# Kernel tuning notes

Measured on AMD Instinct MI355X. Metric: run time of the kernel, lower is better.

## Reference

```python
import jax, jax.numpy as jnp
import numpy as np

B, N, D_IN = 2, 2048, 256
H, DH = 8, 32  # num_heads, head_dim (out_features=256, concat=True)


def setup_inputs() -> dict:
    key = jax.random.key(0)
    ks = jax.random.split(key, 7)
    s = 1.0 / np.sqrt(D_IN)
    x = jax.random.normal(ks[0], (B, N, D_IN), dtype=jnp.float32)
    adj = jax.random.randint(ks[1], (B, N, N), 0, 2).astype(jnp.float32)
    eye = jnp.eye(N, dtype=jnp.float32)[None]
    adj = jnp.maximum(adj, eye)
    Wq = jax.random.normal(ks[2], (H * DH, D_IN), dtype=jnp.float32) * s
    Wk = jax.random.normal(ks[3], (H * DH, D_IN), dtype=jnp.float32) * s
    Wv = jax.random.normal(ks[4], (H * DH, D_IN), dtype=jnp.float32) * s
    Wo = jax.random.normal(ks[5], (H * DH, H * DH), dtype=jnp.float32) * s
    bo = jnp.zeros((H * DH,), dtype=jnp.float32)
    return {"x": x, "adj": adj, "Wq": Wq, "Wk": Wk, "Wv": Wv, "Wo": Wo, "bo": bo}


def reference(x, adj, Wq, Wk, Wv, Wo, bo):
    b, n, _ = x.shape
    # projections -> (b, h, n, dh)
    Q = (x @ Wq.T).reshape(b, n, H, DH).transpose(0, 2, 1, 3)
    K = (x @ Wk.T).reshape(b, n, H, DH).transpose(0, 2, 1, 3)
    V = (x @ Wv.T).reshape(b, n, H, DH).transpose(0, 2, 1, 3)
    scores = jnp.einsum('bhnd,bhmd->bhnm', Q, K) / jnp.sqrt(jnp.float32(DH))
    mask = (adj[:, None, :, :] == 0)  # (b,1,n,n) broadcast over heads
    scores = jnp.where(mask, -jnp.inf, scores)
    attn = jax.nn.softmax(scores, axis=-1)  # dropout is identity in eval
    out = jnp.einsum('bhnm,bhmd->bhnd', attn, V)
    out = out.transpose(0, 2, 1, 3).reshape(b, n, H * DH)  # concat heads
    return out @ Wo.T + bo
```

## Files before the change

### kernel.cpp

```cpp
#include <hip/hip_runtime.h>
#include <hip/hip_bf16.h>

#define BB   2
#define NNN  2048
#define DIN  256
#define HH   8
#define DHD  32
#define NW   32

typedef __attribute__((ext_vector_type(8))) short short8;
typedef __attribute__((ext_vector_type(4))) float f32x4;
typedef __attribute__((ext_vector_type(16))) float f32x16;

#if __has_builtin(__builtin_amdgcn_exp2f)
#define EXP2(x) __builtin_amdgcn_exp2f(x)
#else
#define EXP2(x) exp2f(x)
#endif

__device__ __forceinline__ unsigned int pk2(float a, float b) {
  union { __hip_bfloat162 h2; unsigned int u; } cv;
  cv.h2 = __float22bfloat162_rn(float2{a, b});
  return cv.u;
}
__device__ __forceinline__ unsigned short f2bf(float f) {
  unsigned int u = __float_as_uint(f);
  u += 0x7fffu + ((u >> 16) & 1u);
  return (unsigned short)(u >> 16);
}

#define QSCALE (0.17677669529663687f * 1.4426950408889634f)

__global__ __launch_bounds__(256) void build_mask(
    const float* __restrict__ adj, unsigned long long* __restrict__ Mk,
    const float* __restrict__ Wo, unsigned short* __restrict__ Wob) {
  const int bid = blockIdx.x, tid = threadIdx.x;
  if (bid < 1024) {
    const int lane = tid & 63;
    const int row = bid * 4 + (tid >> 6);
    const float* rp = adj + (size_t)row * NNN + lane * 4;
    #pragma unroll
    for (int o = 0; o < 2; ++o) {
      float4 vv[4];
      #pragma unroll
      for (int g = 0; g < 4; ++g)
        vv[g] = *(const float4*)(rp + (o * 4 + g) * 256);
      #pragma unroll
      for (int g = 0; g < 4; ++g) {
        unsigned long long b0 = __ballot(vv[g].x != 0.0f);
        unsigned long long b1 = __ballot(vv[g].y != 0.0f);
        unsigned long long b2 = __ballot(vv[g].z != 0.0f);
        unsigned long long b3 = __ballot(vv[g].w != 0.0f);
        if (lane < 4) {
          unsigned long long bs = (lane == 0) ? b0 : (lane == 1) ? b1 : (lane == 2) ? b2 : b3;
          Mk[(size_t)row * NW + (o * 4 + g) * 4 + lane] = bs;
        }
      }
    }
  } else {
    int i = (bid - 1024) * 1024 + tid * 4;
    float4 v = *(const float4*)(Wo + i);
    unsigned int p[2] = {pk2(v.x, v.y), pk2(v.z, v.w)};
    *(uint2*)(Wob + i) = *(const uint2*)p;
  }
}

__global__ __launch_bounds__(256) void qkv_gemm(
    const float* __restrict__ x, const float* __restrict__ Wq,
    const float* __restrict__ Wk, const float* __restrict__ Wv,
    unsigned short* __restrict__ Qb, unsigned short* __restrict__ Kb,
    unsigned short* __restrict__ Vt) {
  __shared__ __align__(16) unsigned short Wl[64][264];
  const int tid = threadIdx.x;
  const int y = blockIdx.x >> 6, rb = blockIdx.x & 63;
  const int mat = y >> 2, ocb = (y & 3) * 64;
  const float* Wsrc = ((mat == 0) ? Wq : (mat == 1) ? Wk : Wv) + (size_t)ocb * DIN;

  #pragma unroll
  for (int it = 0; it < 16; ++it) {
    int f4 = it * 256 + tid;
    int oc = f4 >> 6, k4 = f4 & 63;
    float4 v = *(const float4*)(Wsrc + (size_t)oc * DIN + k4 * 4);
    unsigned int p[2] = {pk2(v.x, v.y), pk2(v.z, v.w)};
    *(uint2*)&Wl[oc][k4 * 4] = *(const uint2*)p;
  }
  __syncthreads();

  const int w = tid >> 6, lane = tid & 63, col = lane & 15, quad = lane >> 4;
  const int row0 = rb * 64 + w * 16;

  f32x4 acc[4];
  #pragma unroll
  for (int c = 0; c < 4; ++c) acc[c] = (f32x4){0.f, 0.f, 0.f, 0.f};

  #pragma unroll
  for (int kk = 0; kk < 8; ++kk) {
    const float* xp = x + (size_t)(row0 + col) * DIN + kk * 32 + quad * 8;
    float4 a0 = *(const float4*)xp, a1 = *(const float4*)(xp + 4);
    union { short8 s; unsigned int u[4]; } af;
    af.u[0] = pk2(a0.x, a0.y); af.u[1] = pk2(a0.z, a0.w);
    af.u[2] = pk2(a1.x, a1.y); af.u[3] = pk2(a1.z, a1.w);
    #pragma unroll
    for (int c = 0; c < 4; ++c) {
      short8 bw = *(const short8*)&Wl[c * 16 + col][kk * 32 + quad * 8];
      acc[c] = __builtin_amdgcn_mfma_f32_16x16x32_bf16(af.s, bw, acc[c], 0, 0, 0);
    }
  }
  const float scale = (mat == 0) ? QSCALE : 1.0f;
  #pragma unroll
  for (int c = 0; c < 4; ++c) {
    int oc = ocb + c * 16 + col, h = oc >> 5, dh = oc & 31;
    #pragma unroll
    for (int r = 0; r < 4; ++r) {
      int row = row0 + quad * 4 + r;
      int b = row >> 11, n = row & (NNN - 1);
      unsigned short val = f2bf(acc[c][r] * scale);
      if (mat == 2)       Vt[((size_t)(b * HH + h) * DHD + dh) * NNN + n] = val;
      else if (mat == 0)  Qb[((size_t)(b * HH + h) * NNN + n) * DHD + dh] = val;
      else                Kb[((size_t)(b * HH + h) * NNN + n) * DHD + dh] = val;
    }
  }
}

__global__ __launch_bounds__(512, 6) void attn(
    const unsigned short* __restrict__ Qb, const unsigned short* __restrict__ Kb,
    const unsigned short* __restrict__ Vt, const unsigned long long* __restrict__ Mk,
    unsigned short* __restrict__ AOb) {
  __shared__ float OL[8][32][33];
  __shared__ float LL[8][32];
  const int tid = threadIdx.x;
  const int w = tid >> 6, lane = tid & 63;
  const int qi = lane & 31, hi = lane >> 5;
  const int bid = blockIdx.x;
  const int xcd = bid & 7, j = bid >> 3;
  const int bh = xcd * 2 + (j >> 6);
  const int qt = j & 63;
  const int b = bh >> 3, h = bh & 7;
  const int q = qt * 32 + qi;
  const int k0 = w * 256;

  const unsigned short* qp = Qb + ((size_t)bh * NNN + q) * DHD + hi * 8;
  const short8 bq0 = *(const short8*)qp;
  const short8 bq1 = *(const short8*)(qp + 16);

  f32x16 accO;
  #pragma unroll
  for (int i = 0; i < 16; ++i) accO[i] = 0.f;
  float lsum = 0.f;

  const unsigned long long* mrow = Mk + ((size_t)b * NNN + q) * NW + w * 4;
  unsigned long long bm[4];
  #pragma unroll
  for (int c = 0; c < 4; ++c) bm[c] = mrow[c];

  const unsigned short* kbase = Kb + ((size_t)bh * NNN + k0 + qi) * DHD + hi * 8;
  const unsigned short* vbase = Vt + ((size_t)bh * DHD + qi) * NNN + k0 + hi * 8;

  #pragma unroll 2
  for (int sub = 0; sub < 8; ++sub) {
    const int kb = sub * 32;
    unsigned int mb[4];
    #pragma unroll
    for (int c = 0; c < 4; ++c) mb[c] = (unsigned int)(bm[c] >> (sub * 8)) & 0xffu;

    short8 ak0 = *(const short8*)(kbase + (size_t)kb * DHD);
    short8 ak1 = *(const short8*)(kbase + (size_t)kb * DHD + 16);
    short8 av0 = *(const short8*)(vbase + kb);
    short8 av1 = *(const short8*)(vbase + kb + 16);

    f32x16 z;
    #pragma unroll
    for (int i = 0; i < 16; ++i) z[i] = 0.f;
    f32x16 st = __builtin_amdgcn_mfma_f32_32x32x16_bf16(ak0, bq0, z, 0, 0, 0);
    st = __builtin_amdgcn_mfma_f32_32x32x16_bf16(ak1, bq1, st, 0, 0, 0);

    unsigned int pk[4][2];
    #pragma unroll
    for (int g = 0; g < 4; ++g) {
      float pv[4];
      #pragma unroll
      for (int r = 0; r < 4; ++r) {
        float e = EXP2(st[g * 4 + r]);
        int msk = ((int)(mb[r] << (31 - (g * 2 + hi)))) >> 31;
        float p = __uint_as_float(__float_as_uint(e) & (unsigned int)msk);
        pv[r] = p;
        lsum += p;
      }
      pk[g][0] = pk2(pv[0], pv[1]);
      pk[g][1] = pk2(pv[2], pv[3]);
    }

    unsigned int kA0 = hi ? pk[1][0] : pk[0][0], kA1 = hi ? pk[1][1] : pk[0][1];
    unsigned int tA0 = hi ? pk[0][0] : pk[1][0], tA1 = hi ? pk[0][1] : pk[1][1];
    unsigned int kB0 = hi ? pk[3][0] : pk[2][0], kB1 = hi ? pk[3][1] : pk[2][1];
    unsigned int tB0 = hi ? pk[2][0] : pk[3][0], tB1 = hi ? pk[2][1] : pk[3][1];
    unsigned int xA0 = __shfl_xor((int)tA0, 32, 64), xA1 = __shfl_xor((int)tA1, 32, 64);
    unsigned int xB0 = __shfl_xor((int)tB0, 32, 64), xB1 = __shfl_xor((int)tB1, 32, 64);

    union { short8 s; unsigned int u[4]; } F1, F2;
    F1.u[0] = hi ? xA0 : kA0; F1.u[1] = hi ? xA1 : kA1;
    F1.u[2] = hi ? kA0 : xA0; F1.u[3] = hi ? kA1 : xA1;
    F2.u[0] = hi ? xB0 : kB0; F2.u[1] = hi ? xB1 : kB1;
    F2.u[2] = hi ? kB0 : xB0; F2.u[3] = hi ? kB1 : xB1;

    accO = __builtin_amdgcn_mfma_f32_32x32x16_bf16(av0, F1.s, accO, 0, 0, 0);
    accO = __builtin_amdgcn_mfma_f32_32x32x16_bf16(av1, F2.s, accO, 0, 0, 0);
  }

  lsum += __shfl_xor(lsum, 32, 64);

  #pragma unroll
  for (int g = 0; g < 4; ++g)
    #pragma unroll
    for (int r = 0; r < 4; ++r)
      OL[w][qi][g * 8 + hi * 4 + r] = accO[g * 4 + r];
  if (hi == 0) LL[w][qi] = lsum;
  __syncthreads();

  const int ql = tid >> 4, c2 = (tid & 15) * 2;
  float l = 0.f, o0 = 0.f, o1 = 0.f;
  #pragma unroll
  for (int ww = 0; ww < 8; ++ww) {
    l  += LL[ww][ql];
    o0 += OL[ww][ql][c2];
    o1 += OL[ww][ql][c2 + 1];
  }
  float inv = 1.0f / l;
  unsigned int pr = pk2(o0 * inv, o1 * inv);
  *(unsigned int*)(AOb + ((size_t)(b * NNN + qt * 32 + ql)) * DIN + h * DHD + c2) = pr;
}

__global__ __launch_bounds__(256) void out_proj(const unsigned short* __restrict__ AOb,
                                                const unsigned short* __restrict__ Wob,
                                                const float* __restrict__ bo,
                                                float* __restrict__ out) {
  const int tid = threadIdx.x;
  const int lane = tid & 63, col = lane & 15, quad = lane >> 4;
  const int task = blockIdx.x * 4 + (tid >> 6);
  const int row0 = (task >> 2) * 16;
  const int ocb = (task & 3) * 64;

  f32x4 acc[4];
  #pragma unroll
  for (int c = 0; c < 4; ++c) acc[c] = (f32x4){0.f, 0.f, 0.f, 0.f};

  #pragma unroll
  for (int kk = 0; kk < 8; ++kk) {
    short8 af = *(const short8*)(AOb + (size_t)(row0 + col) * DIN + kk * 32 + quad * 8);
    #pragma unroll
    for (int c = 0; c < 4; ++c) {
      short8 bw = *(const short8*)(Wob + (size_t)(ocb + c * 16 + col) * DIN + kk * 32 + quad * 8);
      acc[c] = __builtin_amdgcn_mfma_f32_16x16x32_bf16(af, bw, acc[c], 0, 0, 0);
    }
  }
  #pragma unroll
  for (int c = 0; c < 4; ++c) {
    int oc = ocb + c * 16 + col;
    float bias = bo[oc];
    #pragma unroll
    for (int r = 0; r < 4; ++r)
      out[(size_t)(row0 + quad * 4 + r) * DIN + oc] = acc[c][r] + bias;
  }
}

extern "C" void kernel_launch(void* const* d_in, const int* in_sizes, int n_in,
                              void* d_out, int out_size, void* d_ws, size_t ws_size,
                              hipStream_t stream) {
  const float* x   = (const float*)d_in[0];
  const float* adj = (const float*)d_in[1];
  const float* Wq  = (const float*)d_in[2];
  const float* Wk  = (const float*)d_in[3];
  const float* Wv  = (const float*)d_in[4];
  const float* Wo  = (const float*)d_in[5];
  const float* bo  = (const float*)d_in[6];
  float* out = (float*)d_out;

  char* ws = (char*)d_ws;
  unsigned short* Qb  = (unsigned short*)(ws);
  unsigned short* Kb  = (unsigned short*)(ws + (2ull << 20));
  unsigned short* Vt  = (unsigned short*)(ws + (4ull << 20));
  unsigned long long* Mk = (unsigned long long*)(ws + (6ull << 20));
  unsigned short* Wob = (unsigned short*)(ws + (7ull << 20));
  unsigned short* AOb = (unsigned short*)(ws + (8ull << 20));

  build_mask<<<dim3(1088), 256, 0, stream>>>(adj, Mk, Wo, Wob);
  qkv_gemm<<<dim3(768), 256, 0, stream>>>(x, Wq, Wk, Wv, Qb, Kb, Vt);
  attn<<<dim3(1024), 512, 0, stream>>>(Qb, Kb, Vt, Mk, AOb);
  out_proj<<<dim3(256), 256, 0, stream>>>(AOb, Wob, bo, out);
}
```

Baseline: 146.9 us.

## Process two query tiles per attention block to reuse K/V fragments

Each attention block now handles 64 queries (two 32-query tiles) instead of 32, so the K and V fragments loaded each iteration feed four MFMAs per tile pair rather than two. The grid is halved to 512 blocks and the launch-bounds occupancy hint drops from 6 to 4 to leave room for the doubled accumulators and mask registers. The goal is to halve K/V global traffic per query. In exchange the kernel uses more registers, has fewer resident waves and blocks, and the LDS reduction is serialized with extra barriers.

```diff
diff --git a/kernel.cpp b/kernel.cpp
--- a/kernel.cpp
+++ b/kernel.cpp
@@ -122,7 +122,7 @@
   }
 }
 
-__global__ __launch_bounds__(512, 6) void attn(
+__global__ __launch_bounds__(512, 4) void attn(
     const unsigned short* __restrict__ Qb, const unsigned short* __restrict__ Kb,
     const unsigned short* __restrict__ Vt, const unsigned long long* __restrict__ Mk,
     unsigned short* __restrict__ AOb) {
@@ -133,25 +133,36 @@
   const int qi = lane & 31, hi = lane >> 5;
   const int bid = blockIdx.x;
   const int xcd = bid & 7, j = bid >> 3;
-  const int bh = xcd * 2 + (j >> 6);
-  const int qt = j & 63;
+  const int bh = xcd * 2 + (j >> 5);
+  const int qg = j & 31;
   const int b = bh >> 3, h = bh & 7;
-  const int q = qt * 32 + qi;
+  const int q0 = qg * 64 + qi;
   const int k0 = w * 256;
 
-  const unsigned short* qp = Qb + ((size_t)bh * NNN + q) * DHD + hi * 8;
-  const short8 bq0 = *(const short8*)qp;
-  const short8 bq1 = *(const short8*)(qp + 16);
-
-  f32x16 accO;
-  #pragma unroll
-  for (int i = 0; i < 16; ++i) accO[i] = 0.f;
-  float lsum = 0.f;
-
-  const unsigned long long* mrow = Mk + ((size_t)b * NNN + q) * NW + w * 4;
-  unsigned long long bm[4];
-  #pragma unroll
-  for (int c = 0; c < 4; ++c) bm[c] = mrow[c];
+  short8 bq[2][2];
+  {
+    const unsigned short* qp0 = Qb + ((size_t)bh * NNN + q0) * DHD + hi * 8;
+    bq[0][0] = *(const short8*)qp0;
+    bq[0][1] = *(const short8*)(qp0 + 16);
+    const unsigned short* qp1 = qp0 + 32 * DHD;
+    bq[1][0] = *(const short8*)qp1;
+    bq[1][1] = *(const short8*)(qp1 + 16);
+  }
+
+  f32x16 accO[2];
+  float lsum[2] = {0.f, 0.f};
+  #pragma unroll
+  for (int tt = 0; tt < 2; ++tt)
+    #pragma unroll
+    for (int i = 0; i < 16; ++i) accO[tt][i] = 0.f;
+
+  unsigned long long bm[2][4];
+  {
+    const unsigned long long* mrow0 = Mk + ((size_t)b * NNN + q0) * NW + w * 4;
+    const unsigned long long* mrow1 = mrow0 + (size_t)32 * NW;
+    #pragma unroll
+    for (int c = 0; c < 4; ++c) { bm[0][c] = mrow0[c]; bm[1][c] = mrow1[c]; }
+  }
 
   const unsigned short* kbase = Kb + ((size_t)bh * NNN + k0 + qi) * DHD + hi * 8;
   const unsigned short* vbase = Vt + ((size_t)bh * DHD + qi) * NNN + k0 + hi * 8;
@@ -159,75 +170,83 @@
   #pragma unroll 2
   for (int sub = 0; sub < 8; ++sub) {
     const int kb = sub * 32;
-    unsigned int mb[4];
-    #pragma unroll
-    for (int c = 0; c < 4; ++c) mb[c] = (unsigned int)(bm[c] >> (sub * 8)) & 0xffu;
-
     short8 ak0 = *(const short8*)(kbase + (size_t)kb * DHD);
     short8 ak1 = *(const short8*)(kbase + (size_t)kb * DHD + 16);
     short8 av0 = *(const short8*)(vbase + kb);
     short8 av1 = *(const short8*)(vbase + kb + 16);
 
-    f32x16 z;
-    #pragma unroll
-    for (int i = 0; i < 16; ++i) z[i] = 0.f;
-    f32x16 st = __builtin_amdgcn_mfma_f32_32x32x16_bf16(ak0, bq0, z, 0, 0, 0);
-    st = __builtin_amdgcn_mfma_f32_32x32x16_bf16(ak1, bq1, st, 0, 0, 0);
-
-    unsigned int pk[4][2];
-    #pragma unroll
-    for (int g = 0; g < 4; ++g) {
-      float pv[4];
-      #pragma unroll
-      for (int r = 0; r < 4; ++r) {
-        float e = EXP2(st[g * 4 + r]);
-        int msk = ((int)(mb[r] << (31 - (g * 2 + hi)))) >> 31;
-        float p = __uint_as_float(__float_as_uint(e) & (unsigned int)msk);
-        pv[r] = p;
-        lsum += p;
+    #pragma unroll
+    for (int tt = 0; tt < 2; ++tt) {
+      unsigned int mb[4];
+      #pragma unroll
+      for (int c = 0; c < 4; ++c) mb[c] = (unsigned int)(bm[tt][c] >> (sub * 8)) & 0xffu;
+
+      f32x16 z;
+      #pragma unroll
+      for (int i = 0; i < 16; ++i) z[i] = 0.f;
+      f32x16 st = __builtin_amdgcn_mfma_f32_32x32x16_bf16(ak0, bq[tt][0], z, 0, 0, 0);
+      st = __builtin_amdgcn_mfma_f32_32x32x16_bf16(ak1, bq[tt][1], st, 0, 0, 0);
+
+      unsigned int pk[4][2];
+      #pragma unroll
+      for (int g = 0; g < 4; ++g) {
+        float pv[4];
+        #pragma unroll
+        for (int r = 0; r < 4; ++r) {
+          float e = EXP2(st[g * 4 + r]);
+          int msk = ((int)(mb[r] << (31 - (g * 2 + hi)))) >> 31;
+          float p = __uint_as_float(__float_as_uint(e) & (unsigned int)msk);
+          pv[r] = p;
+          lsum[tt] += p;
+        }
+        pk[g][0] = pk2(pv[0], pv[1]);
+        pk[g][1] = pk2(pv[2], pv[3]);
       }
-      pk[g][0] = pk2(pv[0], pv[1]);
-      pk[g][1] = pk2(pv[2], pv[3]);
-    }
-
-    unsigned int kA0 = hi ? pk[1][0] : pk[0][0], kA1 = hi ? pk[1][1] : pk[0][1];
-    unsigned int tA0 = hi ? pk[0][0] : pk[1][0], tA1 = hi ? pk[0][1] : pk[1][1];
-    unsigned int kB0 = hi ? pk[3][0] : pk[2][0], kB1 = hi ? pk[3][1] : pk[2][1];
-    unsigned int tB0 = hi ? pk[2][0] : pk[3][0], tB1 = hi ? pk[2][1] : pk[3][1];
-    unsigned int xA0 = __shfl_xor((int)tA0, 32, 64), xA1 = __shfl_xor((int)tA1, 32, 64);
-    unsigned int xB0 = __shfl_xor((int)tB0, 32, 64), xB1 = __shfl_xor((int)tB1, 32, 64);
-
-    union { short8 s; unsigned int u[4]; } F1, F2;
-    F1.u[0] = hi ? xA0 : kA0; F1.u[1] = hi ? xA1 : kA1;
-    F1.u[2] = hi ? kA0 : xA0; F1.u[3] = hi ? kA1 : xA1;
-    F2.u[0] = hi ? xB0 : kB0; F2.u[1] = hi ? xB1 : kB1;
-    F2.u[2] = hi ? kB0 : xB0; F2.u[3] = hi ? kB1 : xB1;
-
-    accO = __builtin_amdgcn_mfma_f32_32x32x16_bf16(av0, F1.s, accO, 0, 0, 0);
-    accO = __builtin_amdgcn_mfma_f32_32x32x16_bf16(av1, F2.s, accO, 0, 0, 0);
-  }
-
-  lsum += __shfl_xor(lsum, 32, 64);
-
-  #pragma unroll
-  for (int g = 0; g < 4; ++g)
-    #pragma unroll
-    for (int r = 0; r < 4; ++r)
-      OL[w][qi][g * 8 + hi * 4 + r] = accO[g * 4 + r];
-  if (hi == 0) LL[w][qi] = lsum;
-  __syncthreads();
-
-  const int ql = tid >> 4, c2 = (tid & 15) * 2;
-  float l = 0.f, o0 = 0.f, o1 = 0.f;
-  #pragma unroll
-  for (int ww = 0; ww < 8; ++ww) {
-    l  += LL[ww][ql];
-    o0 += OL[ww][ql][c2];
-    o1 += OL[ww][ql][c2 + 1];
-  }
-  float inv = 1.0f / l;
-  unsigned int pr = pk2(o0 * inv, o1 * inv);
-  *(unsigned int*)(AOb + ((size_t)(b * NNN + qt * 32 + ql)) * DIN + h * DHD + c2) = pr;
+
+      unsigned int kA0 = hi ? pk[1][0] : pk[0][0], kA1 = hi ? pk[1][1] : pk[0][1];
+      unsigned int tA0 = hi ? pk[0][0] : pk[1][0], tA1 = hi ? pk[0][1] : pk[1][1];
+      unsigned int kB0 = hi ? pk[3][0] : pk[2][0], kB1 = hi ? pk[3][1] : pk[2][1];
+      unsigned int tB0 = hi ? pk[2][0] : pk[3][0], tB1 = hi ? pk[2][1] : pk[3][1];
+      unsigned int xA0 = __shfl_xor((int)tA0, 32, 64), xA1 = __shfl_xor((int)tA1, 32, 64);
+      unsigned int xB0 = __shfl_xor((int)tB0, 32, 64), xB1 = __shfl_xor((int)tB1, 32, 64);
+
+      union { short8 s; unsigned int u[4]; } F1, F2;
+      F1.u[0] = hi ? xA0 : kA0; F1.u[1] = hi ? xA1 : kA1;
+      F1.u[2] = hi ? kA0 : xA0; F1.u[3] = hi ? kA1 : xA1;
+      F2.u[0] = hi ? xB0 : kB0; F2.u[1] = hi ? xB1 : kB1;
+      F2.u[2] = hi ? kB0 : xB0; F2.u[3] = hi ? kB1 : xB1;
+
+      accO[tt] = __builtin_amdgcn_mfma_f32_32x32x16_bf16(av0, F1.s, accO[tt], 0, 0, 0);
+      accO[tt] = __builtin_amdgcn_mfma_f32_32x32x16_bf16(av1, F2.s, accO[tt], 0, 0, 0);
+    }
+  }
+
+  lsum[0] += __shfl_xor(lsum[0], 32, 64);
+  lsum[1] += __shfl_xor(lsum[1], 32, 64);
+
+  #pragma unroll
+  for (int tt = 0; tt < 2; ++tt) {
+    #pragma unroll
+    for (int g = 0; g < 4; ++g)
+      #pragma unroll
+      for (int r = 0; r < 4; ++r)
+        OL[w][qi][g * 8 + hi * 4 + r] = accO[tt][g * 4 + r];
+    if (hi == 0) LL[w][qi] = lsum[tt];
+    __syncthreads();
+
+    const int ql = tid >> 4, c2 = (tid & 15) * 2;
+    float l = 0.f, o0 = 0.f, o1 = 0.f;
+    #pragma unroll
+    for (int ww = 0; ww < 8; ++ww) {
+      l  += LL[ww][ql];
+      o0 += OL[ww][ql][c2];
+      o1 += OL[ww][ql][c2 + 1];
+    }
+    float inv = 1.0f / l;
+    unsigned int pr = pk2(o0 * inv, o1 * inv);
+    *(unsigned int*)(AOb + ((size_t)(b * NNN + qg * 64 + tt * 32 + ql)) * DIN + h * DHD + c2) = pr;
+    __syncthreads();
+  }
 }
 
 __global__ __launch_bounds__(256) void out_proj(const unsigned short* __restrict__ AOb,
@@ -285,6 +304,6 @@
 
   build_mask<<<dim3(1088), 256, 0, stream>>>(adj, Mk, Wo, Wob);
   qkv_gemm<<<dim3(768), 256, 0, stream>>>(x, Wq, Wk, Wv, Qb, Kb, Vt);
-  attn<<<dim3(1024), 512, 0, stream>>>(Qb, Kb, Vt, Mk, AOb);
+  attn<<<dim3(512), 512, 0, stream>>>(Qb, Kb, Vt, Mk, AOb);
   out_proj<<<dim3(256), 256, 0, stream>>>(AOb, Wob, bo, out);
 }
```

After: 162.0 us. 1.1x slower.

## Fuse mask build and QKV projection into one prep kernel; simplify attention mask extraction

Applied to the files above, without the earlier changes.

Merges the adjacency bitmask/Wo conversion kernel and the QKV GEMM into a single launch. The GEMM part now uses 32-column output tiles, giving 1536 GEMM blocks alongside the mask blocks. This removes one launch and lets the bandwidth-bound mask work overlap with the GEMM. In the attention kernel, the mask words are pre-shifted per half-wave, the loop is fully unrolled, and the shuffle/select logic is simplified. The trade-offs are higher register pressure from full unrolling and more redundant x reads in the narrower GEMM tiles.

```diff
diff --git a/kernel.cpp b/kernel.cpp
--- a/kernel.cpp
+++ b/kernel.cpp
@@ -31,13 +31,19 @@
 
 #define QSCALE (0.17677669529663687f * 1.4426950408889634f)
 
-__global__ __launch_bounds__(256) void build_mask(
+__global__ __launch_bounds__(256) void prep(
     const float* __restrict__ adj, unsigned long long* __restrict__ Mk,
+    const float* __restrict__ x, const float* __restrict__ Wq,
+    const float* __restrict__ Wk, const float* __restrict__ Wv,
+    unsigned short* __restrict__ Qb, unsigned short* __restrict__ Kb,
+    unsigned short* __restrict__ Vt,
     const float* __restrict__ Wo, unsigned short* __restrict__ Wob) {
+  __shared__ __align__(16) unsigned short Wl[32][264];
   const int bid = blockIdx.x, tid = threadIdx.x;
+  const int w = tid >> 6, lane = tid & 63;
+
   if (bid < 1024) {
-    const int lane = tid & 63;
-    const int row = bid * 4 + (tid >> 6);
+    const int row = bid * 4 + w;
     const float* rp = adj + (size_t)row * NNN + lane * 4;
     #pragma unroll
     for (int o = 0; o < 2; ++o) {
@@ -57,67 +63,60 @@
         }
       }
     }
-  } else {
+  } else if (bid < 1088) {
     int i = (bid - 1024) * 1024 + tid * 4;
     float4 v = *(const float4*)(Wo + i);
     unsigned int p[2] = {pk2(v.x, v.y), pk2(v.z, v.w)};
     *(uint2*)(Wob + i) = *(const uint2*)p;
-  }
-}
-
-__global__ __launch_bounds__(256) void qkv_gemm(
-    const float* __restrict__ x, const float* __restrict__ Wq,
-    const float* __restrict__ Wk, const float* __restrict__ Wv,
-    unsigned short* __restrict__ Qb, unsigned short* __restrict__ Kb,
-    unsigned short* __restrict__ Vt) {
-  __shared__ __align__(16) unsigned short Wl[64][264];
-  const int tid = threadIdx.x;
-  const int y = blockIdx.x >> 6, rb = blockIdx.x & 63;
-  const int mat = y >> 2, ocb = (y & 3) * 64;
-  const float* Wsrc = ((mat == 0) ? Wq : (mat == 1) ? Wk : Wv) + (size_t)ocb * DIN;
-
-  #pragma unroll
-  for (int it = 0; it < 16; ++it) {
-    int f4 = it * 256 + tid;
-    int oc = f4 >> 6, k4 = f4 & 63;
-    float4 v = *(const float4*)(Wsrc + (size_t)oc * DIN + k4 * 4);
-    unsigned int p[2] = {pk2(v.x, v.y), pk2(v.z, v.w)};
-    *(uint2*)&Wl[oc][k4 * 4] = *(const uint2*)p;
-  }
-  __syncthreads();
-
-  const int w = tid >> 6, lane = tid & 63, col = lane & 15, quad = lane >> 4;
-  const int row0 = rb * 64 + w * 16;
-
-  f32x4 acc[4];
-  #pragma unroll
-  for (int c = 0; c < 4; ++c) acc[c] = (f32x4){0.f, 0.f, 0.f, 0.f};
-
-  #pragma unroll
-  for (int kk = 0; kk < 8; ++kk) {
-    const float* xp = x + (size_t)(row0 + col) * DIN + kk * 32 + quad * 8;
-    float4 a0 = *(const float4*)xp, a1 = *(const float4*)(xp + 4);
-    union { short8 s; unsigned int u[4]; } af;
-    af.u[0] = pk2(a0.x, a0.y); af.u[1] = pk2(a0.z, a0.w);
-    af.u[2] = pk2(a1.x, a1.y); af.u[3] = pk2(a1.z, a1.w);
-    #pragma unroll
-    for (int c = 0; c < 4; ++c) {
-      short8 bw = *(const short8*)&Wl[c * 16 + col][kk * 32 + quad * 8];
-      acc[c] = __builtin_amdgcn_mfma_f32_16x16x32_bf16(af.s, bw, acc[c], 0, 0, 0);
-    }
-  }
-  const float scale = (mat == 0) ? QSCALE : 1.0f;
-  #pragma unroll
-  for (int c = 0; c < 4; ++c) {
-    int oc = ocb + c * 16 + col, h = oc >> 5, dh = oc & 31;
-    #pragma unroll
-    for (int r = 0; r < 4; ++r) {
-      int row = row0 + quad * 4 + r;
-      int b = row >> 11, n = row & (NNN - 1);
-      unsigned short val = f2bf(acc[c][r] * scale);
-      if (mat == 2)       Vt[((size_t)(b * HH + h) * DHD + dh) * NNN + n] = val;
-      else if (mat == 0)  Qb[((size_t)(b * HH + h) * NNN + n) * DHD + dh] = val;
-      else                Kb[((size_t)(b * HH + h) * NNN + n) * DHD + dh] = val;
+  } else {
+    const int t = bid - 1088;
+    const int y = t >> 6, rb = t & 63;
+    const int mat = y >> 3, ocb = (y & 7) * 32;
+    const float* Wsrc = ((mat == 0) ? Wq : (mat == 1) ? Wk : Wv) + (size_t)ocb * DIN;
+
+    #pragma unroll
+    for (int it = 0; it < 8; ++it) {
+      int f4 = it * 256 + tid;
+      int oc = f4 >> 6, k4 = f4 & 63;
+      float4 v = *(const float4*)(Wsrc + (size_t)oc * DIN + k4 * 4);
+      unsigned int p[2] = {pk2(v.x, v.y), pk2(v.z, v.w)};
+      *(uint2*)&Wl[oc][k4 * 4] = *(const uint2*)p;
+    }
+    __syncthreads();
+
+    const int col = lane & 15, quad = lane >> 4;
+    const int row0 = rb * 64 + w * 16;
+
+    f32x4 acc[2];
+    #pragma unroll
+    for (int c = 0; c < 2; ++c) acc[c] = (f32x4){0.f, 0.f, 0.f, 0.f};
+
+    #pragma unroll
+    for (int kk = 0; kk < 8; ++kk) {
+      const float* xp = x + (size_t)(row0 + col) * DIN + kk * 32 + quad * 8;
+      float4 a0 = *(const float4*)xp, a1 = *(const float4*)(xp + 4);
+      union { short8 s; unsigned int u[4]; } af;
+      af.u[0] = pk2(a0.x, a0.y); af.u[1] = pk2(a0.z, a0.w);
+      af.u[2] = pk2(a1.x, a1.y); af.u[3] = pk2(a1.z, a1.w);
+      #pragma unroll
+      for (int c = 0; c < 2; ++c) {
+        short8 bw = *(const short8*)&Wl[c * 16 + col][kk * 32 + quad * 8];
+        acc[c] = __builtin_amdgcn_mfma_f32_16x16x32_bf16(af.s, bw, acc[c], 0, 0, 0);
+      }
+    }
+    const float scale = (mat == 0) ? QSCALE : 1.0f;
+    #pragma unroll
+    for (int c = 0; c < 2; ++c) {
+      int oc = ocb + c * 16 + col, h = oc >> 5, dh = oc & 31;
+      #pragma unroll
+      for (int r = 0; r < 4; ++r) {
+        int row = row0 + quad * 4 + r;
+        int b = row >> 11, n = row & (NNN - 1);
+        unsigned short val = f2bf(acc[c][r] * scale);
+        if (mat == 2)       Vt[((size_t)(b * HH + h) * DHD + dh) * NNN + n] = val;
+        else if (mat == 0)  Qb[((size_t)(b * HH + h) * NNN + n) * DHD + dh] = val;
+        else                Kb[((size_t)(b * HH + h) * NNN + n) * DHD + dh] = val;
+      }
     }
   }
 }
@@ -149,19 +148,20 @@
   float lsum = 0.f;
 
   const unsigned long long* mrow = Mk + ((size_t)b * NNN + q) * NW + w * 4;
-  unsigned long long bm[4];
-  #pragma unroll
-  for (int c = 0; c < 4; ++c) bm[c] = mrow[c];
+  unsigned int mlo[4], mhi2[4];
+  #pragma unroll
+  for (int c = 0; c < 4; ++c) {
+    unsigned long long mh = mrow[c] >> hi;
+    mlo[c]  = (unsigned int)mh;
+    mhi2[c] = (unsigned int)(mh >> 32);
+  }
 
   const unsigned short* kbase = Kb + ((size_t)bh * NNN + k0 + qi) * DHD + hi * 8;
   const unsigned short* vbase = Vt + ((size_t)bh * DHD + qi) * NNN + k0 + hi * 8;
 
-  #pragma unroll 2
+  #pragma unroll
   for (int sub = 0; sub < 8; ++sub) {
     const int kb = sub * 32;
-    unsigned int mb[4];
-    #pragma unroll
-    for (int c = 0; c < 4; ++c) mb[c] = (unsigned int)(bm[c] >> (sub * 8)) & 0xffu;
 
     short8 ak0 = *(const short8*)(kbase + (size_t)kb * DHD);
     short8 ak1 = *(const short8*)(kbase + (size_t)kb * DHD + 16);
@@ -180,8 +180,10 @@
       float pv[4];
       #pragma unroll
       for (int r = 0; r < 4; ++r) {
+        unsigned int mwd = (sub < 4) ? mlo[r] : mhi2[r];
+        const int pos = (sub & 3) * 8 + g * 2;
+        int msk = ((int)(mwd << (31 - pos))) >> 31;
         float e = EXP2(st[g * 4 + r]);
-        int msk = ((int)(mb[r] << (31 - (g * 2 + hi)))) >> 31;
         float p = __uint_as_float(__float_as_uint(e) & (unsigned int)msk);
         pv[r] = p;
         lsum += p;
@@ -190,18 +192,20 @@
       pk[g][1] = pk2(pv[2], pv[3]);
     }
 
-    unsigned int kA0 = hi ? pk[1][0] : pk[0][0], kA1 = hi ? pk[1][1] : pk[0][1];
-    unsigned int tA0 = hi ? pk[0][0] : pk[1][0], tA1 = hi ? pk[0][1] : pk[1][1];
-    unsigned int kB0 = hi ? pk[3][0] : pk[2][0], kB1 = hi ? pk[3][1] : pk[2][1];
-    unsigned int tB0 = hi ? pk[2][0] : pk[3][0], tB1 = hi ? pk[2][1] : pk[3][1];
-    unsigned int xA0 = __shfl_xor((int)tA0, 32, 64), xA1 = __shfl_xor((int)tA1, 32, 64);
-    unsigned int xB0 = __shfl_xor((int)tB0, 32, 64), xB1 = __shfl_xor((int)tB1, 32, 64);
+    unsigned int x00 = __shfl_xor((int)pk[0][0], 32, 64), x01 = __shfl_xor((int)pk[0][1], 32, 64);
+    unsigned int x10 = __shfl_xor((int)pk[1][0], 32, 64), x11 = __shfl_xor((int)pk[1][1], 32, 64);
+    unsigned int x20 = __shfl_xor((int)pk[2][0], 32, 64), x21 = __shfl_xor((int)pk[2][1], 32, 64);
+    unsigned int x30 = __shfl_xor((int)pk[3][0], 32, 64), x31 = __shfl_xor((int)pk[3][1], 32, 64);
 
     union { short8 s; unsigned int u[4]; } F1, F2;
-    F1.u[0] = hi ? xA0 : kA0; F1.u[1] = hi ? xA1 : kA1;
-    F1.u[2] = hi ? kA0 : xA0; F1.u[3] = hi ? kA1 : xA1;
-    F2.u[0] = hi ? xB0 : kB0; F2.u[1] = hi ? xB1 : kB1;
-    F2.u[2] = hi ? kB0 : xB0; F2.u[3] = hi ? kB1 : xB1;
+    F1.u[0] = hi ? x10 : pk[0][0];
+    F1.u[1] = hi ? x11 : pk[0][1];
+    F1.u[2] = hi ? pk[1][0] : x00;
+    F1.u[3] = hi ? pk[1][1] : x01;
+    F2.u[0] = hi ? x30 : pk[2][0];
+    F2.u[1] = hi ? x31 : pk[2][1];
+    F2.u[2] = hi ? pk[3][0] : x20;
+    F2.u[3] = hi ? pk[3][1] : x21;
 
     accO = __builtin_amdgcn_mfma_f32_32x32x16_bf16(av0, F1.s, accO, 0, 0, 0);
     accO = __builtin_amdgcn_mfma_f32_32x32x16_bf16(av1, F2.s, accO, 0, 0, 0);
@@ -283,8 +287,7 @@
   unsigned short* Wob = (unsigned short*)(ws + (7ull << 20));
   unsigned short* AOb = (unsigned short*)(ws + (8ull << 20));
 
-  build_mask<<<dim3(1088), 256, 0, stream>>>(adj, Mk, Wo, Wob);
-  qkv_gemm<<<dim3(768), 256, 0, stream>>>(x, Wq, Wk, Wv, Qb, Kb, Vt);
+  prep<<<dim3(2624), 256, 0, stream>>>(adj, Mk, x, Wq, Wk, Wv, Qb, Kb, Vt, Wo, Wob);
   attn<<<dim3(1024), 512, 0, stream>>>(Qb, Kb, Vt, Mk, AOb);
   out_proj<<<dim3(256), 256, 0, stream>>>(AOb, Wob, bo, out);
 }
```

New measurement: 139.7 us. -4.9%, faster.
